# Optimization experiments

Measured on AMD Instinct MI355X. Metric: run time of the kernel, lower is better.

## Reference

```python
import jax, jax.numpy as jnp
import numpy as np

N_NODES = 100000
N_EDGES = 1600000
D_FEAT = 48
K = 10
ALPHA = 0.1


def setup_inputs() -> dict:
    key = jax.random.key(0)
    k1, k2, k3 = jax.random.split(key, 3)
    x = jax.random.normal(k1, (N_NODES, D_FEAT), dtype=jnp.float32)
    edge_index = jax.random.randint(k2, (2, N_EDGES), 0, N_NODES, dtype=jnp.int64)
    edge_weight = jax.random.uniform(k3, (N_EDGES,), dtype=jnp.float32)
    return {"x": x, "edge_index": edge_index, "edge_weight": edge_weight}


def reference(x, edge_index, edge_weight):
    row, col = edge_index[0], edge_index[1]
    # degree-weighted normalization: w_ij / sum_j w_ij
    deg_w = jax.ops.segment_sum(edge_weight, row, num_segments=N_NODES)
    norm = edge_weight / (deg_w[row] + 1e-10)  # [E]

    def step(h, _):
        # gather h at source-of-message (col), scale, scatter-add to row
        msg = jax.ops.segment_sum(norm[:, None] * h[col], row, num_segments=N_NODES)
        h_new = (1.0 - ALPHA) * msg + ALPHA * x
        return h_new, None

    h, _ = jax.lax.scan(step, x, None, length=K)
    return h
```

## Files before the change

kernel.cpp:

```cpp
#include <hip/hip_runtime.h>
#include <hip/hip_fp16.h>

#define N_NODES 100000
#define N_EDGES 1600000
#define K_ITER 10

#define TPN 6
#define NPB 32
#define PAD 4
#define RS 8

#define SCAN_TB   256
#define SCAN_EPT  8
#define SCAN_SEG  (SCAN_TB * SCAN_EPT)
#define SCAN_NB   ((N_NODES + SCAN_SEG - 1) / SCAN_SEG)

typedef unsigned int u32;

__global__ void k_count(const int* __restrict__ row, u32* __restrict__ cnt2,
                        unsigned char* __restrict__ pos_local, int E) {
    int i = blockIdx.x * blockDim.x + threadIdx.x;
    if (i < E) {
        int r = row[i];
        u32 inc = (r & 1) ? 0x10000u : 1u;
        u32 old = atomicAdd(&cnt2[r >> 1], inc);
        pos_local[i] = (unsigned char)((old >> ((r & 1) * 16)) & 0xffffu);
    }
}

__device__ __forceinline__ int padded_cnt(const u32* cnt2, int i) {
    int cv = (int)((cnt2[i >> 1] >> ((i & 1) * 16)) & 0xffffu);
    return (cv + (PAD - 1)) & ~(PAD - 1);
}

__global__ void k_scanA(const u32* __restrict__ cnt2, int* __restrict__ thread_off,
                        int* __restrict__ blocksum) {
    __shared__ int sh[SCAN_TB];
    int b = blockIdx.x, t = threadIdx.x;
    int base = b * SCAN_SEG + t * SCAN_EPT;
    int s = 0;
#pragma unroll
    for (int j = 0; j < SCAN_EPT; ++j) {
        int i = base + j;
        if (i < N_NODES) s += padded_cnt(cnt2, i);
    }
    sh[t] = s;
    __syncthreads();
    for (int off = 1; off < SCAN_TB; off <<= 1) {
        int v = (t >= off) ? sh[t - off] : 0;
        __syncthreads();
        sh[t] += v;
        __syncthreads();
    }
    thread_off[b * SCAN_TB + t] = sh[t] - s;
    if (t == SCAN_TB - 1) blocksum[b] = sh[t];
}

__global__ void k_scanB(const int* __restrict__ blocksum, int* __restrict__ blockoff,
                        int* __restrict__ rowptr) {
    __shared__ int sh[SCAN_TB];
    int t = threadIdx.x;
    int v = (t < SCAN_NB) ? blocksum[t] : 0;
    sh[t] = v;
    __syncthreads();
    for (int off = 1; off < SCAN_TB; off <<= 1) {
        int u = (t >= off) ? sh[t - off] : 0;
        __syncthreads();
        sh[t] += u;
        __syncthreads();
    }
    if (t < SCAN_NB) blockoff[t] = sh[t] - v;
    if (t == SCAN_NB - 1) rowptr[N_NODES] = sh[t];
}

__global__ void k_scanC(const u32* __restrict__ cnt2, const int* __restrict__ thread_off,
                        const int* __restrict__ blockoff, int* __restrict__ rowptr) {
    int b = blockIdx.x, t = threadIdx.x;
    int base = b * SCAN_SEG + t * SCAN_EPT;
    int run = blockoff[b] + thread_off[b * SCAN_TB + t];
#pragma unroll
    for (int j = 0; j < SCAN_EPT; ++j) {
        int i = base + j;
        if (i < N_NODES) {
            rowptr[i] = run;
            run += padded_cnt(cnt2, i);
        }
    }
}

__global__ void k_fill(const int* __restrict__ row, const int* __restrict__ col,
                       const float* __restrict__ w, const int* __restrict__ rowptr,
                       const unsigned char* __restrict__ pos_local,
                       u32* __restrict__ epack, int E) {
    int i = blockIdx.x * blockDim.x + threadIdx.x;
    if (i < E) {
        int pos = rowptr[row[i]] + (int)pos_local[i];
        epack[pos] = ((u32)col[i] << 15) | (__float_as_uint(w[i]) >> 17);
    }
}

__global__ void k_scale(const int* __restrict__ rowptr, const u32* __restrict__ epack,
                        float* __restrict__ scale) {
    int n = blockIdx.x * blockDim.x + threadIdx.x;
    if (n >= N_NODES) return;
    int beg = rowptr[n], end = rowptr[n + 1];
    float s = 0.f;
    for (int e = beg; e < end; ++e)
        s += __uint_as_float((epack[e] & 0x7fffu) << 17);
    scale[n] = 0.9f / (s + 1e-10f);
}

__global__ void k_x2h(const float4* __restrict__ x, float4* __restrict__ x16) {
    int i = blockIdx.x * blockDim.x + threadIdx.x;
    int n = i / TPN, c = i % TPN;
    if (n >= N_NODES) return;
    float4 a = x[n * 12 + 2 * c], b = x[n * 12 + 2 * c + 1];
    float4 o;
    ((__half2*)&o)[0] = __floats2half2_rn(a.x, a.y);
    ((__half2*)&o)[1] = __floats2half2_rn(a.z, a.w);
    ((__half2*)&o)[2] = __floats2half2_rn(b.x, b.y);
    ((__half2*)&o)[3] = __floats2half2_rn(b.z, b.w);
    x16[(n << 3) + c] = o;
}

#define GFMA(UJ, AA, BB)                                                      \
    {                                                                         \
        u32 uu = (UJ);                                                        \
        float4 hv = src16[((uu >> 15) << 3) + c];                             \
        float wv = __uint_as_float((uu & 0x7fffu) << 17) * sc;                \
        float2 f0 = __half22float2(*(__half2*)&hv.x);                         \
        float2 f1 = __half22float2(*(__half2*)&hv.y);                         \
        float2 f2 = __half22float2(*(__half2*)&hv.z);                         \
        float2 f3 = __half22float2(*(__half2*)&hv.w);                         \
        AA.x += wv * f0.x; AA.y += wv * f0.y; AA.z += wv * f1.x; AA.w += wv * f1.y; \
        BB.x += wv * f2.x; BB.y += wv * f2.y; BB.z += wv * f3.x; BB.w += wv * f3.y; \
    }

template <int LAST>
__global__ __launch_bounds__(192) void k_pull(const int* __restrict__ rowptr,
                                              const u32* __restrict__ epack,
                                              const float* __restrict__ scale,
                                              const float4* __restrict__ x,
                                              const float4* __restrict__ src16,
                                              void* __restrict__ dstv) {
    int node = blockIdx.x * NPB + threadIdx.x / TPN;
    int c = threadIdx.x % TPN;
    if (node >= N_NODES) return;
    int beg = rowptr[node], end = rowptr[node + 1];
    float sc = scale[node];
    float4 xa = x[node * 12 + 2 * c], xb = x[node * 12 + 2 * c + 1];
    float4 A0 = make_float4(0.1f * xa.x, 0.1f * xa.y, 0.1f * xa.z, 0.1f * xa.w);
    float4 B0 = make_float4(0.1f * xb.x, 0.1f * xb.y, 0.1f * xb.z, 0.1f * xb.w);
    float4 A1 = make_float4(0, 0, 0, 0), B1 = make_float4(0, 0, 0, 0);
    for (int e = beg; e < end; e += 4) {
        uint4 p = *(const uint4*)(epack + e);
        GFMA(p.x, A0, B0) GFMA(p.y, A1, B1)
        GFMA(p.z, A0, B0) GFMA(p.w, A1, B1)
    }
    float4 RA = make_float4(A0.x + A1.x, A0.y + A1.y, A0.z + A1.z, A0.w + A1.w);
    float4 RB = make_float4(B0.x + B1.x, B0.y + B1.y, B0.z + B1.z, B0.w + B1.w);
    if (LAST) {
        float4* out = (float4*)dstv;
        out[node * 12 + 2 * c]     = RA;
        out[node * 12 + 2 * c + 1] = RB;
    } else {
        float4 o;
        ((__half2*)&o)[0] = __floats2half2_rn(RA.x, RA.y);
        ((__half2*)&o)[1] = __floats2half2_rn(RA.z, RA.w);
        ((__half2*)&o)[2] = __floats2half2_rn(RB.x, RB.y);
        ((__half2*)&o)[3] = __floats2half2_rn(RB.z, RB.w);
        ((float4*)dstv)[(node << 3) + c] = o;
    }
}

extern "C" void kernel_launch(void* const* d_in, const int* in_sizes, int n_in,
                              void* d_out, int out_size, void* d_ws, size_t ws_size,
                              hipStream_t stream) {
    const float* x  = (const float*)d_in[0];
    const int*   ei = (const int*)d_in[1];
    const float* w  = (const float*)d_in[2];
    const int E = in_sizes[2];
    const int* row = ei;
    const int* col = ei + E;

    char* ws = (char*)d_ws;
    int*           rowptr     = (int*)(ws);
    u32*           epack      = (u32*)(ws + 400016);
    float*         scale      = (float*)(ws + 8000096);
    int*           thread_off = (int*)(ws + 8400096);
    int*           blocksum   = (int*)(ws + 8450272);
    int*           blockoff   = (int*)(ws + 8451296);
    u32*           cnt2       = (u32*)(ws + 8452320);
    unsigned char* pos_local  = (unsigned char*)(ws + 8652320);
    float4*        hB16       = (float4*)(ws + 10252320);
    float4*        hA16       = (float4*)d_out;

    const int B = 256;
    const int egrid = (E + B - 1) / B;
    const int ngrid = (N_NODES + B - 1) / B;
    const int pgrid = N_NODES / NPB;
    const int xgrid = (N_NODES * TPN + 191) / 192;

    hipMemsetAsync(cnt2, 0, (N_NODES / 2) * sizeof(u32), stream);
    hipMemsetAsync(epack, 0, (size_t)(E + 3 * N_NODES + 16) * sizeof(u32), stream);
    k_count<<<egrid, B, 0, stream>>>(row, cnt2, pos_local, E);
    k_scanA<<<SCAN_NB, SCAN_TB, 0, stream>>>(cnt2, thread_off, blocksum);
    k_scanB<<<1, SCAN_TB, 0, stream>>>(blocksum, blockoff, rowptr);
    k_scanC<<<SCAN_NB, SCAN_TB, 0, stream>>>(cnt2, thread_off, blockoff, rowptr);
    k_fill <<<egrid, B, 0, stream>>>(row, col, w, rowptr, pos_local, epack, E);
    k_scale<<<ngrid, B, 0, stream>>>(rowptr, epack, scale);
    k_x2h  <<<xgrid, 192, 0, stream>>>((const float4*)x, hA16);

    float4* src = hA16;
    float4* dst = hB16;
    for (int k = 1; k <= K_ITER - 1; ++k) {
        k_pull<0><<<pgrid, NPB * TPN, 0, stream>>>(rowptr, epack, scale,
                                                   (const float4*)x, src, dst);
        float4* t = src; src = dst; dst = t;
    }
    k_pull<1><<<pgrid, NPB * TPN, 0, stream>>>(rowptr, epack, scale,
                                               (const float4*)x, src, d_out);
}
```

Baseline: 499.7 us.

## Spread atomic counters, pad rows to 8 edges, unroll pull loop with nontemporal loads

The per-node degree counters are spread to a 32-byte stride so neighbouring nodes no longer share a word in the counting atomics. Row padding grows from 4 to 8 edges, and the pull loop now reads two 16-byte edge chunks per step into four accumulator pairs, which gives more memory-level parallelism. Edge and x reads use nontemporal loads to keep them from displacing the gathered features in cache. The cost is more padded zero edges to process, a larger counter buffer to clear, and more registers per thread.

Result: slower. 528.9 us (+5.8%).

```diff
diff --git a/kernel.cpp b/kernel.cpp
--- a/kernel.cpp
+++ b/kernel.cpp
@@ -7,8 +7,8 @@
 
 #define TPN 6
 #define NPB 32
-#define PAD 4
-#define RS 8
+#define PAD 8
+#define CSTRIDE 8
 
 #define SCAN_TB   256
 #define SCAN_EPT  8
@@ -16,24 +16,21 @@
 #define SCAN_NB   ((N_NODES + SCAN_SEG - 1) / SCAN_SEG)
 
 typedef unsigned int u32;
-
-__global__ void k_count(const int* __restrict__ row, u32* __restrict__ cnt2,
+typedef u32   u32x4 __attribute__((ext_vector_type(4)));
+typedef float f32x4 __attribute__((ext_vector_type(4)));
+
+__global__ void k_count(const int* __restrict__ row, u32* __restrict__ cnt,
                         unsigned char* __restrict__ pos_local, int E) {
     int i = blockIdx.x * blockDim.x + threadIdx.x;
-    if (i < E) {
-        int r = row[i];
-        u32 inc = (r & 1) ? 0x10000u : 1u;
-        u32 old = atomicAdd(&cnt2[r >> 1], inc);
-        pos_local[i] = (unsigned char)((old >> ((r & 1) * 16)) & 0xffffu);
-    }
-}
-
-__device__ __forceinline__ int padded_cnt(const u32* cnt2, int i) {
-    int cv = (int)((cnt2[i >> 1] >> ((i & 1) * 16)) & 0xffffu);
+    if (i < E) pos_local[i] = (unsigned char)atomicAdd(&cnt[row[i] << 3], 1u);
+}
+
+__device__ __forceinline__ int padded_cnt(const u32* cnt, int i) {
+    int cv = (int)cnt[i << 3];
     return (cv + (PAD - 1)) & ~(PAD - 1);
 }
 
-__global__ void k_scanA(const u32* __restrict__ cnt2, int* __restrict__ thread_off,
+__global__ void k_scanA(const u32* __restrict__ cnt, int* __restrict__ thread_off,
                         int* __restrict__ blocksum) {
     __shared__ int sh[SCAN_TB];
     int b = blockIdx.x, t = threadIdx.x;
@@ -42,7 +39,7 @@
 #pragma unroll
     for (int j = 0; j < SCAN_EPT; ++j) {
         int i = base + j;
-        if (i < N_NODES) s += padded_cnt(cnt2, i);
+        if (i < N_NODES) s += padded_cnt(cnt, i);
     }
     sh[t] = s;
     __syncthreads();
@@ -73,7 +70,7 @@
     if (t == SCAN_NB - 1) rowptr[N_NODES] = sh[t];
 }
 
-__global__ void k_scanC(const u32* __restrict__ cnt2, const int* __restrict__ thread_off,
+__global__ void k_scanC(const u32* __restrict__ cnt, const int* __restrict__ thread_off,
                         const int* __restrict__ blockoff, int* __restrict__ rowptr) {
     int b = blockIdx.x, t = threadIdx.x;
     int base = b * SCAN_SEG + t * SCAN_EPT;
@@ -83,7 +80,7 @@
         int i = base + j;
         if (i < N_NODES) {
             rowptr[i] = run;
-            run += padded_cnt(cnt2, i);
+            run += padded_cnt(cnt, i);
         }
     }
 }
@@ -140,7 +137,7 @@
 __global__ __launch_bounds__(192) void k_pull(const int* __restrict__ rowptr,
                                               const u32* __restrict__ epack,
                                               const float* __restrict__ scale,
-                                              const float4* __restrict__ x,
+                                              const float* __restrict__ x,
                                               const float4* __restrict__ src16,
                                               void* __restrict__ dstv) {
     int node = blockIdx.x * NPB + threadIdx.x / TPN;
@@ -148,17 +145,27 @@
     if (node >= N_NODES) return;
     int beg = rowptr[node], end = rowptr[node + 1];
     float sc = scale[node];
-    float4 xa = x[node * 12 + 2 * c], xb = x[node * 12 + 2 * c + 1];
+    const f32x4* xp = (const f32x4*)(x + node * 48 + c * 8);
+    f32x4 xa = __builtin_nontemporal_load(xp);
+    f32x4 xb = __builtin_nontemporal_load(xp + 1);
     float4 A0 = make_float4(0.1f * xa.x, 0.1f * xa.y, 0.1f * xa.z, 0.1f * xa.w);
     float4 B0 = make_float4(0.1f * xb.x, 0.1f * xb.y, 0.1f * xb.z, 0.1f * xb.w);
     float4 A1 = make_float4(0, 0, 0, 0), B1 = make_float4(0, 0, 0, 0);
-    for (int e = beg; e < end; e += 4) {
-        uint4 p = *(const uint4*)(epack + e);
-        GFMA(p.x, A0, B0) GFMA(p.y, A1, B1)
-        GFMA(p.z, A0, B0) GFMA(p.w, A1, B1)
-    }
-    float4 RA = make_float4(A0.x + A1.x, A0.y + A1.y, A0.z + A1.z, A0.w + A1.w);
-    float4 RB = make_float4(B0.x + B1.x, B0.y + B1.y, B0.z + B1.z, B0.w + B1.w);
+    float4 A2 = make_float4(0, 0, 0, 0), B2 = make_float4(0, 0, 0, 0);
+    float4 A3 = make_float4(0, 0, 0, 0), B3 = make_float4(0, 0, 0, 0);
+    for (int e = beg; e < end; e += 8) {
+        const u32x4* ep = (const u32x4*)(epack + e);
+        u32x4 pa = __builtin_nontemporal_load(ep);
+        u32x4 pb = __builtin_nontemporal_load(ep + 1);
+        GFMA(pa.x, A0, B0) GFMA(pa.y, A1, B1)
+        GFMA(pa.z, A2, B2) GFMA(pa.w, A3, B3)
+        GFMA(pb.x, A0, B0) GFMA(pb.y, A1, B1)
+        GFMA(pb.z, A2, B2) GFMA(pb.w, A3, B3)
+    }
+    float4 RA = make_float4(A0.x + A1.x + A2.x + A3.x, A0.y + A1.y + A2.y + A3.y,
+                            A0.z + A1.z + A2.z + A3.z, A0.w + A1.w + A2.w + A3.w);
+    float4 RB = make_float4(B0.x + B1.x + B2.x + B3.x, B0.y + B1.y + B2.y + B3.y,
+                            B0.z + B1.z + B2.z + B3.z, B0.w + B1.w + B2.w + B3.w);
     if (LAST) {
         float4* out = (float4*)dstv;
         out[node * 12 + 2 * c]     = RA;
@@ -186,13 +193,13 @@
     char* ws = (char*)d_ws;
     int*           rowptr     = (int*)(ws);
     u32*           epack      = (u32*)(ws + 400016);
-    float*         scale      = (float*)(ws + 8000096);
-    int*           thread_off = (int*)(ws + 8400096);
-    int*           blocksum   = (int*)(ws + 8450272);
-    int*           blockoff   = (int*)(ws + 8451296);
-    u32*           cnt2       = (u32*)(ws + 8452320);
-    unsigned char* pos_local  = (unsigned char*)(ws + 8652320);
-    float4*        hB16       = (float4*)(ws + 10252320);
+    float*         scale      = (float*)(ws + 9600096);
+    int*           thread_off = (int*)(ws + 10000096);
+    int*           blocksum   = (int*)(ws + 10050272);
+    int*           blockoff   = (int*)(ws + 10051296);
+    u32*           cntS       = (u32*)(ws + 10052352);
+    unsigned char* pos_local  = (unsigned char*)(ws + 13252352);
+    float4*        hB16       = (float4*)(ws + 14852352);
     float4*        hA16       = (float4*)d_out;
 
     const int B = 256;
@@ -201,12 +208,12 @@
     const int pgrid = N_NODES / NPB;
     const int xgrid = (N_NODES * TPN + 191) / 192;
 
-    hipMemsetAsync(cnt2, 0, (N_NODES / 2) * sizeof(u32), stream);
-    hipMemsetAsync(epack, 0, (size_t)(E + 3 * N_NODES + 16) * sizeof(u32), stream);
-    k_count<<<egrid, B, 0, stream>>>(row, cnt2, pos_local, E);
-    k_scanA<<<SCAN_NB, SCAN_TB, 0, stream>>>(cnt2, thread_off, blocksum);
+    hipMemsetAsync(cntS, 0, (size_t)N_NODES * CSTRIDE * sizeof(u32), stream);
+    hipMemsetAsync(epack, 0, (size_t)(N_EDGES + 7 * N_NODES + 16) * sizeof(u32), stream);
+    k_count<<<egrid, B, 0, stream>>>(row, cntS, pos_local, E);
+    k_scanA<<<SCAN_NB, SCAN_TB, 0, stream>>>(cntS, thread_off, blocksum);
     k_scanB<<<1, SCAN_TB, 0, stream>>>(blocksum, blockoff, rowptr);
-    k_scanC<<<SCAN_NB, SCAN_TB, 0, stream>>>(cnt2, thread_off, blockoff, rowptr);
+    k_scanC<<<SCAN_NB, SCAN_TB, 0, stream>>>(cntS, thread_off, blockoff, rowptr);
     k_fill <<<egrid, B, 0, stream>>>(row, col, w, rowptr, pos_local, epack, E);
     k_scale<<<ngrid, B, 0, stream>>>(rowptr, epack, scale);
     k_x2h  <<<xgrid, 192, 0, stream>>>((const float4*)x, hA16);
@@ -215,9 +222,9 @@
     float4* dst = hB16;
     for (int k = 1; k <= K_ITER - 1; ++k) {
         k_pull<0><<<pgrid, NPB * TPN, 0, stream>>>(rowptr, epack, scale,
-                                                   (const float4*)x, src, dst);
+                                                   x, src, dst);
         float4* t = src; src = dst; dst = t;
     }
     k_pull<1><<<pgrid, NPB * TPN, 0, stream>>>(rowptr, epack, scale,
-                                               (const float4*)x, src, d_out);
-}
+                                               x, src, d_out);
+}
```
